# Kernel optimization log

Measured on AMD Instinct MI355X. Metric: run time of the kernel, lower is better.

Reference implementation:

```python
import jax, jax.numpy as jnp
import numpy as np

N = 100000
E = 1_600_000
IN_CH = 64
HID = 32       # per-head hidden dim
HEADS = 4
OUT_CH = 6
NEG_SLOPE = 0.2


def _glorot(key, shape):
    fan_in, fan_out = shape[0], shape[-1]
    lim = jnp.sqrt(6.0 / (fan_in + fan_out))
    return jax.random.uniform(key, shape, jnp.float32, -lim, lim)


def setup_inputs() -> dict:
    key = jax.random.key(0)
    ks = jax.random.split(key, 20)
    x = jax.random.normal(ks[0], (N, IN_CH), jnp.float32)
    edge_index = jax.random.randint(ks[1], (2, E), 0, N, jnp.int64)
    batch = jnp.zeros((N,), jnp.int64)
    inp = {"x": x, "edge_index": edge_index, "batch": batch}
    inp["W0"] = _glorot(ks[2], (IN_CH, HEADS * HID))
    inp["as0"] = _glorot(ks[3], (HEADS, HID))
    inp["ad0"] = _glorot(ks[4], (HEADS, HID))
    inp["b0"] = jnp.zeros((HEADS * HID,), jnp.float32)
    inp["W1"] = _glorot(ks[5], (HEADS * HID, HEADS * HID))
    inp["as1"] = _glorot(ks[6], (HEADS, HID))
    inp["ad1"] = _glorot(ks[7], (HEADS, HID))
    inp["b1"] = jnp.zeros((HEADS * HID,), jnp.float32)
    inp["W2"] = _glorot(ks[8], (HEADS * HID, HEADS * HID))
    inp["as2"] = _glorot(ks[9], (HEADS, HID))
    inp["ad2"] = _glorot(ks[10], (HEADS, HID))
    inp["b2"] = jnp.zeros((HEADS * HID,), jnp.float32)
    # final layer: 128 -> 6, 1 head, no concat (mean)
    inp["W3"] = _glorot(ks[11], (HEADS * HID, OUT_CH))
    inp["as3"] = _glorot(ks[12], (1, OUT_CH))
    inp["ad3"] = _glorot(ks[13], (1, OUT_CH))
    inp["b3"] = jnp.zeros((OUT_CH,), jnp.float32)
    return inp


def gat_conv(x, src, dst, W, a_src, a_dst, b, heads, concat):
    """PyG GATConv: linear -> per-edge attention -> segment softmax over dst -> scatter-add."""
    n = x.shape[0]
    h = (x @ W).reshape(n, heads, -1)                       # [N,H,D]
    al_s = jnp.sum(h * a_src, axis=-1)                      # [N,H]
    al_d = jnp.sum(h * a_dst, axis=-1)                      # [N,H]
    e = jax.nn.leaky_relu(al_s[src] + al_d[dst], NEG_SLOPE)  # [E,H]
    m = jax.ops.segment_max(e, dst, num_segments=n)         # segment softmax (stable)
    ex = jnp.exp(e - m[dst])
    s = jax.ops.segment_sum(ex, dst, num_segments=n)
    alpha = ex / (s[dst] + 1e-16)                           # [E,H]
    out = jax.ops.segment_sum(alpha[:, :, None] * h[src], dst, num_segments=n)  # [N,H,D]
    out = out.reshape(n, -1) if concat else out.mean(axis=1)
    return out + b


def reference(x, edge_index, batch, W0, as0, ad0, b0, W1, as1, ad1, b1,
              W2, as2, ad2, b2, W3, as3, ad3, b3):
    n = x.shape[0]
    # PyG GATConv adds self-loops by default; edge set is static (no pooling), add once.
    ar = jnp.arange(n, dtype=edge_index.dtype)
    ei = jnp.concatenate([edge_index, jnp.stack([ar, ar])], axis=1)
    src, dst = ei[0], ei[1]
    x = jax.nn.elu(gat_conv(x, src, dst, W0, as0, ad0, b0, HEADS, True))
    x = jax.nn.elu(gat_conv(x, src, dst, W1, as1, ad1, b1, HEADS, True))
    x = jax.nn.elu(gat_conv(x, src, dst, W2, as2, ad2, b2, HEADS, True))
    x = gat_conv(x, src, dst, W3, as3, ad3, b3, 1, False)   # final layer: no activation
    return x
```

## Files before the change

kernel.cpp:

```cpp
#include <hip/hip_runtime.h>
#include <hip/hip_bf16.h>
#include <hip/hip_fp16.h>

#define IN_CH 64
#define HID 32
#define HEADS 4
#define OUT_CH 6
#define NEG_SLOPE 0.2f


#define PBLK 256
#define CAP 6144

__global__ __launch_bounds__(256) void part_count(const int* __restrict__ ei, int E, int EN,
                                                  int NB, int epb, int* __restrict__ counts) {
    __shared__ int cnt[512];
    int b = blockIdx.x, t = threadIdx.x;
    for (int i = t; i < NB; i += 256) cnt[i] = 0;
    __syncthreads();
    int e0 = b * epb;
    int e1 = min(e0 + epb, EN);
    for (int e = e0 + t; e < e1; e += 256) {
        int d = (e < E) ? ei[E + e] : (e - E);
        atomicAdd(&cnt[d >> 8], 1);
    }
    __syncthreads();
    for (int i = t; i < NB; i += 256) counts[(size_t)i * PBLK + b] = cnt[i];
}

__global__ __launch_bounds__(256) void bucket_tot(const int* __restrict__ counts,
                                                  int* __restrict__ btot) {
    __shared__ int red[256];
    int k = blockIdx.x, t = threadIdx.x;
    red[t] = counts[(size_t)k * PBLK + t];
    __syncthreads();
    for (int off = 128; off; off >>= 1) {
        if (t < off) red[t] += red[t + off];
        __syncthreads();
    }
    if (t == 0) btot[k] = red[0];
}

__global__ __launch_bounds__(256) void bucket_scan(const int* __restrict__ btot, int NB, int EN,
                                                   int* __restrict__ bstart) {
    __shared__ int tmp[256];
    int t = threadIdx.x;
    int chunk = (NB + 255) >> 8;
    int s0 = t * chunk, s1 = min(s0 + chunk, NB);
    int sum = 0;
    for (int i = s0; i < s1; ++i) sum += btot[i];
    tmp[t] = sum;
    __syncthreads();
    for (int off = 1; off < 256; off <<= 1) {
        int v = (t >= off) ? tmp[t - off] : 0;
        __syncthreads();
        tmp[t] += v;
        __syncthreads();
    }
    int run = (t == 0) ? 0 : tmp[t - 1];
    for (int i = s0; i < s1; ++i) {
        int c = btot[i];
        bstart[i] = run;
        run += c;
    }
    if (t == 255) bstart[NB] = EN;
}

__global__ __launch_bounds__(256) void bucket_base(int* __restrict__ counts,
                                                   const int* __restrict__ bstart) {
    __shared__ int sc[256];
    int k = blockIdx.x, t = threadIdx.x;
    int v = counts[(size_t)k * PBLK + t];
    sc[t] = v;
    __syncthreads();
    for (int off = 1; off < 256; off <<= 1) {
        int u = (t >= off) ? sc[t - off] : 0;
        __syncthreads();
        sc[t] += u;
        __syncthreads();
    }
    counts[(size_t)k * PBLK + t] = bstart[k] + sc[t] - v;
}

__global__ __launch_bounds__(256) void part_scatter(const int* __restrict__ ei, int E, int EN,
                                                    int NB, int epb,
                                                    const int* __restrict__ base,
                                                    int2* __restrict__ ebuf) {
    __shared__ int cur[512];
    int b = blockIdx.x, t = threadIdx.x;
    for (int i = t; i < NB; i += 256) cur[i] = base[(size_t)i * PBLK + b];
    __syncthreads();
    int e0 = b * epb;
    int e1 = min(e0 + epb, EN);
    for (int e = e0 + t; e < e1; e += 256) {
        int s, d;
        if (e < E) { s = ei[e]; d = ei[E + e]; }
        else       { s = e - E; d = s; }
        int slot = atomicAdd(&cur[d >> 8], 1);
        ebuf[slot] = make_int2(s, d & 255);
    }
}

__global__ __launch_bounds__(256) void bucket_csr(const int2* __restrict__ ebuf,
                                                  const int* __restrict__ bstart,
                                                  int NB, int N, int EN,
                                                  int* __restrict__ row_start,
                                                  int* __restrict__ csr_src) {
    __shared__ int cnt[256];
    __shared__ int sc[256];
    __shared__ int stage[CAP];
    int k = blockIdx.x, t = threadIdx.x;
    int s0 = bstart[k], s1 = bstart[k + 1];
    int len = s1 - s0;
    cnt[t] = 0;
    __syncthreads();
    for (int i = t; i < len; i += 256) atomicAdd(&cnt[ebuf[s0 + i].y], 1);
    __syncthreads();
    int v = cnt[t];
    sc[t] = v;
    __syncthreads();
    for (int off = 1; off < 256; off <<= 1) {
        int u = (t >= off) ? sc[t - off] : 0;
        __syncthreads();
        sc[t] += u;
        __syncthreads();
    }
    int excl = sc[t] - v;
    int g = (k << 8) + t;
    if (g < N) row_start[g] = s0 + excl;
    if (k == NB - 1 && t == 0) row_start[N] = EN;
    bool fits = (len <= CAP);
    cnt[t] = fits ? excl : s0 + excl;
    __syncthreads();
    if (fits) {
        for (int i = t; i < len; i += 256) {
            int2 e = ebuf[s0 + i];
            int slot = atomicAdd(&cnt[e.y], 1);
            stage[slot] = e.x;
        }
        __syncthreads();
        for (int i = t; i < len; i += 256) csr_src[s0 + i] = stage[i];
    } else {
        for (int i = t; i < len; i += 256) {
            int2 e = ebuf[s0 + i];
            int slot = atomicAdd(&cnt[e.y], 1);
            csr_src[slot] = e.x;
        }
    }
}


#define BM 32
#define BKK 32

__global__ __launch_bounds__(256) void gemm128_kernel(const float* __restrict__ A,
                                                      const float* __restrict__ W,
                                                      const float* __restrict__ avs,
                                                      const float* __restrict__ avd,
                                                      __half* __restrict__ C,
                                                      float* __restrict__ als,
                                                      float* __restrict__ ald,
                                                      int N, int K) {
    __shared__ float xs[BM][BKK + 1];
    __shared__ float ws[BKK][128];
    __shared__ float red_s[BM][9];
    __shared__ float red_d[BM][9];
    int tid = threadIdx.x;
    int r  = tid & 31;
    int cg = tid >> 5;
    int row0 = blockIdx.x * BM;

    float acc[16];
#pragma unroll
    for (int j = 0; j < 16; ++j) acc[j] = 0.f;

    for (int kk = 0; kk < K; kk += BKK) {
        {
            int lr = tid >> 3, lc = (tid & 7) * 4;
            int gr = row0 + lr;
            float4 v = make_float4(0.f, 0.f, 0.f, 0.f);
            if (gr < N) v = *reinterpret_cast<const float4*>(A + (size_t)gr * K + kk + lc);
            xs[lr][lc + 0] = v.x; xs[lr][lc + 1] = v.y;
            xs[lr][lc + 2] = v.z; xs[lr][lc + 3] = v.w;
        }
        {
            int wr = tid >> 3, wc = (tid & 7) * 16;
            const float4* src = reinterpret_cast<const float4*>(W + (size_t)(kk + wr) * 128 + wc);
            float4* dst = reinterpret_cast<float4*>(&ws[wr][wc]);
#pragma unroll
            for (int i = 0; i < 4; ++i) dst[i] = src[i];
        }
        __syncthreads();
#pragma unroll 8
        for (int k = 0; k < BKK; ++k) {
            float xv = xs[r][k];
            const float4* wrow = reinterpret_cast<const float4*>(&ws[k][cg * 16]);
#pragma unroll
            for (int q = 0; q < 4; ++q) {
                float4 wv = wrow[q];
                acc[q * 4 + 0] += xv * wv.x;
                acc[q * 4 + 1] += xv * wv.y;
                acc[q * 4 + 2] += xv * wv.z;
                acc[q * 4 + 3] += xv * wv.w;
            }
        }
        __syncthreads();
    }
    int gr = row0 + r;
    if (gr < N) {
        __half2* outp = reinterpret_cast<__half2*>(C + (size_t)gr * 128 + cg * 16);
#pragma unroll
        for (int q = 0; q < 8; ++q)
            outp[q] = __float22half2_rn(make_float2(acc[q * 2], acc[q * 2 + 1]));
    }
    {
        float ps = 0.f, pd = 0.f;
#pragma unroll
        for (int q = 0; q < 16; ++q) {
            float a = acc[q];
            ps += a * avs[cg * 16 + q];
            pd += a * avd[cg * 16 + q];
        }
        red_s[r][cg] = ps;
        red_d[r][cg] = pd;
        __syncthreads();
        if (gr < N) {
            if (cg < 4) {
                als[(size_t)gr * 4 + cg] = red_s[r][2 * cg] + red_s[r][2 * cg + 1];
            } else {
                int hd = cg - 4;
                ald[(size_t)gr * 4 + hd] = red_d[r][2 * hd] + red_d[r][2 * hd + 1];
            }
        }
    }
}


__device__ __forceinline__ float lrelu(float x) { return x > 0.f ? x : NEG_SLOPE * x; }

__global__ __launch_bounds__(256) void agg_kernel(const __half* __restrict__ h,
                                                  const float* __restrict__ als4,
                                                  const float* __restrict__ ald4,
                                                  const int* __restrict__ row_start,
                                                  const int* __restrict__ csr_src,
                                                  const float* __restrict__ bias,
                                                  float* __restrict__ xout,
                                                  int N, int applyElu) {
    int v = (int)((blockIdx.x * blockDim.x + threadIdx.x) >> 6);
    int lane = threadIdx.x & 63;
    if (v >= N) return;
    int base = row_start[v], end = row_start[v + 1];

    int half_ = lane >> 5;
    int dim4 = (lane & 31) * 4;
    int hd2  = (lane & 31) >> 3;

    float aldh = ald4[(size_t)v * 4 + hd2];
    float alsh = als4[(size_t)v * 4 + hd2];
    float em = lrelu(alsh + aldh);
    const __half* hdim = h + dim4;
    const float* alsb = als4 + hd2;

    float4 acc  = make_float4(0.f, 0.f, 0.f, 0.f);
    float4 acc2 = make_float4(0.f, 0.f, 0.f, 0.f);
    float ssum = 0.f, ssum2 = 0.f;

    int j = base + half_;
    for (; j + 6 < end; j += 8) {
        int s0 = csr_src[j + 0];
        int s1 = csr_src[j + 2];
        int s2 = csr_src[j + 4];
        int s3 = csr_src[j + 6];
        float a0 = alsb[(size_t)s0 * 4];
        float a1 = alsb[(size_t)s1 * 4];
        float a2 = alsb[(size_t)s2 * 4];
        float a3 = alsb[(size_t)s3 * 4];
        uint2 r0 = *reinterpret_cast<const uint2*>(hdim + (size_t)s0 * 128);
        uint2 r1 = *reinterpret_cast<const uint2*>(hdim + (size_t)s1 * 128);
        uint2 r2 = *reinterpret_cast<const uint2*>(hdim + (size_t)s2 * 128);
        uint2 r3 = *reinterpret_cast<const uint2*>(hdim + (size_t)s3 * 128);
        float e0 = __expf(lrelu(a0 + aldh) - em);
        float e1 = __expf(lrelu(a1 + aldh) - em);
        float e2 = __expf(lrelu(a2 + aldh) - em);
        float e3 = __expf(lrelu(a3 + aldh) - em);
        ssum  += e0 + e2;
        ssum2 += e1 + e3;
        float2 f0a = __half22float2(*reinterpret_cast<__half2*>(&r0.x));
        float2 f0b = __half22float2(*reinterpret_cast<__half2*>(&r0.y));
        float2 f1a = __half22float2(*reinterpret_cast<__half2*>(&r1.x));
        float2 f1b = __half22float2(*reinterpret_cast<__half2*>(&r1.y));
        float2 f2a = __half22float2(*reinterpret_cast<__half2*>(&r2.x));
        float2 f2b = __half22float2(*reinterpret_cast<__half2*>(&r2.y));
        float2 f3a = __half22float2(*reinterpret_cast<__half2*>(&r3.x));
        float2 f3b = __half22float2(*reinterpret_cast<__half2*>(&r3.y));
        acc.x  += e0 * f0a.x; acc.y  += e0 * f0a.y; acc.z  += e0 * f0b.x; acc.w  += e0 * f0b.y;
        acc2.x += e1 * f1a.x; acc2.y += e1 * f1a.y; acc2.z += e1 * f1b.x; acc2.w += e1 * f1b.y;
        acc.x  += e2 * f2a.x; acc.y  += e2 * f2a.y; acc.z  += e2 * f2b.x; acc.w  += e2 * f2b.y;
        acc2.x += e3 * f3a.x; acc2.y += e3 * f3a.y; acc2.z += e3 * f3b.x; acc2.w += e3 * f3b.y;
    }
    for (; j < end; j += 2) {
        int s0 = csr_src[j];
        float a0 = alsb[(size_t)s0 * 4];
        uint2 r0 = *reinterpret_cast<const uint2*>(hdim + (size_t)s0 * 128);
        float e0 = __expf(lrelu(a0 + aldh) - em);
        ssum += e0;
        float2 f0a = __half22float2(*reinterpret_cast<__half2*>(&r0.x));
        float2 f0b = __half22float2(*reinterpret_cast<__half2*>(&r0.y));
        acc.x += e0 * f0a.x; acc.y += e0 * f0a.y; acc.z += e0 * f0b.x; acc.w += e0 * f0b.y;
    }
    acc.x += acc2.x; acc.y += acc2.y; acc.z += acc2.z; acc.w += acc2.w;
    ssum += ssum2;
    acc.x += __shfl_xor(acc.x, 32);
    acc.y += __shfl_xor(acc.y, 32);
    acc.z += __shfl_xor(acc.z, 32);
    acc.w += __shfl_xor(acc.w, 32);
    ssum  += __shfl_xor(ssum, 32);

    if (lane < 32) {
        float inv = 1.0f / (ssum + 1e-16f);
        float4 bv = *reinterpret_cast<const float4*>(bias + dim4);
        float4 o;
        o.x = acc.x * inv + bv.x;
        o.y = acc.y * inv + bv.y;
        o.z = acc.z * inv + bv.z;
        o.w = acc.w * inv + bv.w;
        if (applyElu) {
            o.x = o.x > 0.f ? o.x : expm1f(o.x);
            o.y = o.y > 0.f ? o.y : expm1f(o.y);
            o.z = o.z > 0.f ? o.z : expm1f(o.z);
            o.w = o.w > 0.f ? o.w : expm1f(o.w);
        }
        *reinterpret_cast<float4*>(xout + (size_t)v * 128 + dim4) = o;
    }
}


__global__ void gemm3_kernel(const float* __restrict__ x, const float* __restrict__ W,
                             const float* __restrict__ as3, const float* __restrict__ ad3,
                             float* __restrict__ h3, float* __restrict__ als3,
                             float* __restrict__ ald3, int N) {
    int n = blockIdx.x * blockDim.x + threadIdx.x;
    if (n >= N) return;
    float acc[6] = {0.f, 0.f, 0.f, 0.f, 0.f, 0.f};
    const float4* xp = reinterpret_cast<const float4*>(x + (size_t)n * 128);
#pragma unroll 4
    for (int k4 = 0; k4 < 32; ++k4) {
        float4 xv = xp[k4];
        const float* w0 = W + (size_t)(k4 * 4) * 6;
#pragma unroll
        for (int j = 0; j < 6; ++j)
            acc[j] += xv.x * w0[j] + xv.y * w0[6 + j] + xv.z * w0[12 + j] + xv.w * w0[18 + j];
    }
    float s = 0.f, d = 0.f;
#pragma unroll
    for (int j = 0; j < 6; ++j) {
        s += acc[j] * as3[j];
        d += acc[j] * ad3[j];
        h3[(size_t)n * 6 + j] = acc[j];
    }
    als3[n] = s;
    ald3[n] = d;
}

__global__ void agg3_kernel(const float* __restrict__ h3, const float* __restrict__ als3,
                            const float* __restrict__ ald3, const int* __restrict__ row_start,
                            const int* __restrict__ csr_src, const float* __restrict__ b3,
                            float* __restrict__ out, int N) {
    int v = blockIdx.x * blockDim.x + threadIdx.x;
    if (v >= N) return;
    int base = row_start[v], end = row_start[v + 1];
    float aldv = ald3[v];
    float em = lrelu(als3[v] + aldv);
    float ssum = 0.f;
    float acc[6] = {0.f, 0.f, 0.f, 0.f, 0.f, 0.f};
    float acc2[6] = {0.f, 0.f, 0.f, 0.f, 0.f, 0.f};
    int j = base;
    for (; j + 1 < end; j += 2) {
        int sa = csr_src[j], sb = csr_src[j + 1];
        float ea = __expf(lrelu(als3[sa] + aldv) - em);
        float eb = __expf(lrelu(als3[sb] + aldv) - em);
        ssum += ea + eb;
        const float* ha = h3 + (size_t)sa * 6;
        const float* hb = h3 + (size_t)sb * 6;
#pragma unroll
        for (int q = 0; q < 6; ++q) acc[q] += ea * ha[q];
#pragma unroll
        for (int q = 0; q < 6; ++q) acc2[q] += eb * hb[q];
    }
    if (j < end) {
        int sa = csr_src[j];
        float ea = __expf(lrelu(als3[sa] + aldv) - em);
        ssum += ea;
        const float* ha = h3 + (size_t)sa * 6;
#pragma unroll
        for (int q = 0; q < 6; ++q) acc[q] += ea * ha[q];
    }
    float inv = 1.f / (ssum + 1e-16f);
#pragma unroll
    for (int q = 0; q < 6; ++q) out[(size_t)v * 6 + q] = (acc[q] + acc2[q]) * inv + b3[q];
}


extern "C" void kernel_launch(void* const* d_in, const int* in_sizes, int n_in,
                              void* d_out, int out_size, void* d_ws, size_t ws_size,
                              hipStream_t stream) {
    const float* x    = (const float*)d_in[0];
    const int*   ei   = (const int*)d_in[1];
    const float* W0   = (const float*)d_in[3];
    const float* as0  = (const float*)d_in[4];
    const float* ad0  = (const float*)d_in[5];
    const float* b0   = (const float*)d_in[6];
    const float* W1   = (const float*)d_in[7];
    const float* as1  = (const float*)d_in[8];
    const float* ad1  = (const float*)d_in[9];
    const float* b1   = (const float*)d_in[10];
    const float* W2   = (const float*)d_in[11];
    const float* as2  = (const float*)d_in[12];
    const float* ad2  = (const float*)d_in[13];
    const float* b2   = (const float*)d_in[14];
    const float* W3   = (const float*)d_in[15];
    const float* as3  = (const float*)d_in[16];
    const float* ad3  = (const float*)d_in[17];
    const float* b3   = (const float*)d_in[18];
    float* out = (float*)d_out;

    int N = in_sizes[0] / IN_CH;
    int E = in_sizes[1] / 2;
    int EN = E + N;
    int NB = (N + 255) >> 8;
    int epb = (EN + PBLK - 1) / PBLK;

    char* p = (char*)d_ws;
    auto alloc = [&](size_t bytes) {
        char* q = p;
        p += (bytes + 255) & ~(size_t)255;
        return q;
    };
    __half* hbuf = (__half*)alloc((size_t)N * 128 * 2);
    float* xA   = (float*)alloc((size_t)N * 128 * 4);
    float* xB   = (float*)alloc((size_t)N * 128 * 4);
    float* als  = (float*)alloc((size_t)N * 4 * 4);
    float* ald  = (float*)alloc((size_t)N * 4 * 4);
    float* h3   = (float*)alloc((size_t)N * 6 * 4);
    float* als3 = (float*)alloc((size_t)N * 4);
    float* ald3 = (float*)alloc((size_t)N * 4);
    int* row_start = (int*)alloc((size_t)(N + 1) * 4);
    int* csr_src   = (int*)alloc((size_t)EN * 4);
    int2* ebuf     = (int2*)alloc((size_t)EN * 8);
    int* counts    = (int*)alloc((size_t)NB * PBLK * 4);
    int* btot      = (int*)alloc((size_t)NB * 4);
    int* bstart    = (int*)alloc((size_t)(NB + 1) * 4);
    (void)ws_size; (void)n_in; (void)out_size;

    part_count<<<PBLK, 256, 0, stream>>>(ei, E, EN, NB, epb, counts);
    bucket_tot<<<NB, 256, 0, stream>>>(counts, btot);
    bucket_scan<<<1, 256, 0, stream>>>(btot, NB, EN, bstart);
    bucket_base<<<NB, 256, 0, stream>>>(counts, bstart);
    part_scatter<<<PBLK, 256, 0, stream>>>(ei, E, EN, NB, epb, counts, ebuf);
    bucket_csr<<<NB, 256, 0, stream>>>(ebuf, bstart, NB, N, EN, row_start, csr_src);

    int gemm_grid = (N + BM - 1) / BM;
    int agg_grid  = (N + 3) / 4;
    int n_grid    = (N + 255) / 256;

    gemm128_kernel<<<gemm_grid, 256, 0, stream>>>(x, W0, as0, ad0, hbuf, als, ald, N, 64);
    agg_kernel<<<agg_grid, 256, 0, stream>>>(hbuf, als, ald, row_start, csr_src, b0, xA, N, 1);

    gemm128_kernel<<<gemm_grid, 256, 0, stream>>>(xA, W1, as1, ad1, hbuf, als, ald, N, 128);
    agg_kernel<<<agg_grid, 256, 0, stream>>>(hbuf, als, ald, row_start, csr_src, b1, xB, N, 1);

    gemm128_kernel<<<gemm_grid, 256, 0, stream>>>(xB, W2, as2, ad2, hbuf, als, ald, N, 128);
    agg_kernel<<<agg_grid, 256, 0, stream>>>(hbuf, als, ald, row_start, csr_src, b2, xA, N, 1);

    gemm3_kernel<<<n_grid, 256, 0, stream>>>(xA, W3, as3, ad3, h3, als3, ald3, N);
    agg3_kernel<<<n_grid, 256, 0, stream>>>(h3, als3, ald3, row_start, csr_src, b3, out, N);
}
```

Measured before the change: 521.5 us.

## Use 8x4 register tiles and transposed A tile in 128-wide GEMM

Reworks the node-feature GEMM so each thread computes an 8-row by 4-column register tile over a 64-row block, with the A tile stored transposed in shared memory for vectorised float4 reads. The attention-logit reductions now use warp shuffles instead of a shared-memory reduction and an extra barrier. The aim is more FMAs per shared-memory load and a lower LDS-to-compute ratio. The trade-off is higher register pressure and fewer blocks, since the block now covers 64 rows.

New measurement: 458.2 us. 1.14x faster.

```diff
diff --git a/kernel.cpp b/kernel.cpp
--- a/kernel.cpp
+++ b/kernel.cpp
@@ -150,8 +150,9 @@
 }
 
 
-#define BM 32
-#define BKK 32
+#define GBM 64
+#define GBK 32
+#define XST 68
 
 __global__ __launch_bounds__(256) void gemm128_kernel(const float* __restrict__ A,
                                                       const float* __restrict__ W,
@@ -161,75 +162,91 @@
                                                       float* __restrict__ als,
                                                       float* __restrict__ ald,
                                                       int N, int K) {
-    __shared__ float xs[BM][BKK + 1];
-    __shared__ float ws[BKK][128];
-    __shared__ float red_s[BM][9];
-    __shared__ float red_d[BM][9];
+    __shared__ float xsT[GBK][XST];
+    __shared__ float ws[GBK][128];
     int tid = threadIdx.x;
-    int r  = tid & 31;
-    int cg = tid >> 5;
-    int row0 = blockIdx.x * BM;
-
-    float acc[16];
-#pragma unroll
-    for (int j = 0; j < 16; ++j) acc[j] = 0.f;
-
-    for (int kk = 0; kk < K; kk += BKK) {
+    int rt = tid >> 5;
+    int ct = tid & 31;
+    int row0 = blockIdx.x * GBM;
+
+    float acc[8][4];
+#pragma unroll
+    for (int i = 0; i < 8; ++i)
+#pragma unroll
+        for (int j = 0; j < 4; ++j) acc[i][j] = 0.f;
+
+    int arow = tid & 63;
+    int acg  = (tid >> 6) * 8;
+    int garow = row0 + arow;
+
+    for (int kk = 0; kk < K; kk += GBK) {
         {
-            int lr = tid >> 3, lc = (tid & 7) * 4;
-            int gr = row0 + lr;
-            float4 v = make_float4(0.f, 0.f, 0.f, 0.f);
-            if (gr < N) v = *reinterpret_cast<const float4*>(A + (size_t)gr * K + kk + lc);
-            xs[lr][lc + 0] = v.x; xs[lr][lc + 1] = v.y;
-            xs[lr][lc + 2] = v.z; xs[lr][lc + 3] = v.w;
+            float4 a0 = make_float4(0.f, 0.f, 0.f, 0.f);
+            float4 a1 = make_float4(0.f, 0.f, 0.f, 0.f);
+            if (garow < N) {
+                const float4* ap = reinterpret_cast<const float4*>(A + (size_t)garow * K + kk + acg);
+                a0 = ap[0]; a1 = ap[1];
+            }
+            xsT[acg + 0][arow] = a0.x; xsT[acg + 1][arow] = a0.y;
+            xsT[acg + 2][arow] = a0.z; xsT[acg + 3][arow] = a0.w;
+            xsT[acg + 4][arow] = a1.x; xsT[acg + 5][arow] = a1.y;
+            xsT[acg + 6][arow] = a1.z; xsT[acg + 7][arow] = a1.w;
         }
         {
-            int wr = tid >> 3, wc = (tid & 7) * 16;
-            const float4* src = reinterpret_cast<const float4*>(W + (size_t)(kk + wr) * 128 + wc);
-            float4* dst = reinterpret_cast<float4*>(&ws[wr][wc]);
-#pragma unroll
-            for (int i = 0; i < 4; ++i) dst[i] = src[i];
-        }
-        __syncthreads();
-#pragma unroll 8
-        for (int k = 0; k < BKK; ++k) {
-            float xv = xs[r][k];
-            const float4* wrow = reinterpret_cast<const float4*>(&ws[k][cg * 16]);
-#pragma unroll
-            for (int q = 0; q < 4; ++q) {
-                float4 wv = wrow[q];
-                acc[q * 4 + 0] += xv * wv.x;
-                acc[q * 4 + 1] += xv * wv.y;
-                acc[q * 4 + 2] += xv * wv.z;
-                acc[q * 4 + 3] += xv * wv.w;
+            float4* wflat = reinterpret_cast<float4*>(&ws[0][0]);
+            const float4* wsrc = reinterpret_cast<const float4*>(W + (size_t)kk * 128);
+#pragma unroll
+            for (int c = 0; c < 4; ++c) {
+                int p = tid + 256 * c;
+                wflat[p] = wsrc[p];
             }
         }
         __syncthreads();
-    }
-    int gr = row0 + r;
-    if (gr < N) {
-        __half2* outp = reinterpret_cast<__half2*>(C + (size_t)gr * 128 + cg * 16);
-#pragma unroll
-        for (int q = 0; q < 8; ++q)
-            outp[q] = __float22half2_rn(make_float2(acc[q * 2], acc[q * 2 + 1]));
-    }
-    {
-        float ps = 0.f, pd = 0.f;
-#pragma unroll
-        for (int q = 0; q < 16; ++q) {
-            float a = acc[q];
-            ps += a * avs[cg * 16 + q];
-            pd += a * avd[cg * 16 + q];
-        }
-        red_s[r][cg] = ps;
-        red_d[r][cg] = pd;
-        __syncthreads();
+#pragma unroll 4
+        for (int k = 0; k < GBK; ++k) {
+            float4 av0 = *reinterpret_cast<const float4*>(&xsT[k][rt * 8]);
+            float4 av1 = *reinterpret_cast<const float4*>(&xsT[k][rt * 8 + 4]);
+            float4 wv  = *reinterpret_cast<const float4*>(&ws[k][ct * 4]);
+            acc[0][0] += av0.x * wv.x; acc[0][1] += av0.x * wv.y; acc[0][2] += av0.x * wv.z; acc[0][3] += av0.x * wv.w;
+            acc[1][0] += av0.y * wv.x; acc[1][1] += av0.y * wv.y; acc[1][2] += av0.y * wv.z; acc[1][3] += av0.y * wv.w;
+            acc[2][0] += av0.z * wv.x; acc[2][1] += av0.z * wv.y; acc[2][2] += av0.z * wv.z; acc[2][3] += av0.z * wv.w;
+            acc[3][0] += av0.w * wv.x; acc[3][1] += av0.w * wv.y; acc[3][2] += av0.w * wv.z; acc[3][3] += av0.w * wv.w;
+            acc[4][0] += av1.x * wv.x; acc[4][1] += av1.x * wv.y; acc[4][2] += av1.x * wv.z; acc[4][3] += av1.x * wv.w;
+            acc[5][0] += av1.y * wv.x; acc[5][1] += av1.y * wv.y; acc[5][2] += av1.y * wv.z; acc[5][3] += av1.y * wv.w;
+            acc[6][0] += av1.z * wv.x; acc[6][1] += av1.z * wv.y; acc[6][2] += av1.z * wv.z; acc[6][3] += av1.z * wv.w;
+            acc[7][0] += av1.w * wv.x; acc[7][1] += av1.w * wv.y; acc[7][2] += av1.w * wv.z; acc[7][3] += av1.w * wv.w;
+        }
+        __syncthreads();
+    }
+
+#pragma unroll
+    for (int i = 0; i < 8; ++i) {
+        int gr = row0 + rt * 8 + i;
         if (gr < N) {
-            if (cg < 4) {
-                als[(size_t)gr * 4 + cg] = red_s[r][2 * cg] + red_s[r][2 * cg + 1];
-            } else {
-                int hd = cg - 4;
-                ald[(size_t)gr * 4 + hd] = red_d[r][2 * hd] + red_d[r][2 * hd + 1];
+            __half2* outp = reinterpret_cast<__half2*>(C + (size_t)gr * 128 + ct * 4);
+            outp[0] = __float22half2_rn(make_float2(acc[i][0], acc[i][1]));
+            outp[1] = __float22half2_rn(make_float2(acc[i][2], acc[i][3]));
+        }
+    }
+    float avs_c[4], avd_c[4];
+#pragma unroll
+    for (int j = 0; j < 4; ++j) {
+        avs_c[j] = avs[ct * 4 + j];
+        avd_c[j] = avd[ct * 4 + j];
+    }
+#pragma unroll
+    for (int i = 0; i < 8; ++i) {
+        float ps = acc[i][0] * avs_c[0] + acc[i][1] * avs_c[1] + acc[i][2] * avs_c[2] + acc[i][3] * avs_c[3];
+        float pd = acc[i][0] * avd_c[0] + acc[i][1] * avd_c[1] + acc[i][2] * avd_c[2] + acc[i][3] * avd_c[3];
+        ps += __shfl_xor(ps, 1); pd += __shfl_xor(pd, 1);
+        ps += __shfl_xor(ps, 2); pd += __shfl_xor(pd, 2);
+        ps += __shfl_xor(ps, 4); pd += __shfl_xor(pd, 4);
+        if ((ct & 7) == 0) {
+            int gr = row0 + rt * 8 + i;
+            int hd = ct >> 3;
+            if (gr < N) {
+                als[(size_t)gr * 4 + hd] = ps;
+                ald[(size_t)gr * 4 + hd] = pd;
             }
         }
     }
@@ -459,7 +476,7 @@
     part_scatter<<<PBLK, 256, 0, stream>>>(ei, E, EN, NB, epb, counts, ebuf);
     bucket_csr<<<NB, 256, 0, stream>>>(ebuf, bstart, NB, N, EN, row_start, csr_src);
 
-    int gemm_grid = (N + BM - 1) / BM;
+    int gemm_grid = (N + GBM - 1) / GBM;
     int agg_grid  = (N + 3) / 4;
     int n_grid    = (N + 255) / 256;
 
```

## Use fp16 MFMA for node-feature GEMMs and store activations in half precision

Applied to the files above, without the earlier changes.

Replaces the fp32 scalar-FMA GEMM with a 16x16x32 fp16 MFMA kernel. Each wave loads its A-fragments straight from global memory and reads weights that a small kernel has pre-transposed and converted to fp16. Aggregation outputs and the layer-0 input are now stored in fp16, which halves activation traffic for the GEMMs and for gemm3. The attention logit dot products are reduced with wave shuffles. This costs extra precision loss, a few small conversion kernels, and uncoalesced scalar fp16 stores of C.

After: 445.8 us. -14.5%, faster.

```diff
diff --git a/kernel.cpp b/kernel.cpp
--- a/kernel.cpp
+++ b/kernel.cpp
@@ -7,6 +7,9 @@
 #define HEADS 4
 #define OUT_CH 6
 #define NEG_SLOPE 0.2f
+
+typedef __attribute__((ext_vector_type(8))) _Float16 half8;
+typedef __attribute__((ext_vector_type(4))) float f32x4;
 
 
 #define PBLK 256
@@ -150,86 +153,122 @@
 }
 
 
-#define BM 32
-#define BKK 32
-
-__global__ __launch_bounds__(256) void gemm128_kernel(const float* __restrict__ A,
-                                                      const float* __restrict__ W,
-                                                      const float* __restrict__ avs,
-                                                      const float* __restrict__ avd,
-                                                      __half* __restrict__ C,
-                                                      float* __restrict__ als,
-                                                      float* __restrict__ ald,
-                                                      int N, int K) {
-    __shared__ float xs[BM][BKK + 1];
-    __shared__ float ws[BKK][128];
-    __shared__ float red_s[BM][9];
-    __shared__ float red_d[BM][9];
+__global__ void xconv_kernel(const float* __restrict__ x, __half* __restrict__ xh, int total4) {
+    int t = blockIdx.x * blockDim.x + threadIdx.x;
+    if (t >= total4) return;
+    float4 v = *reinterpret_cast<const float4*>(x + (size_t)t * 4);
+    __half2* op = reinterpret_cast<__half2*>(xh + (size_t)t * 4);
+    op[0] = __float22half2_rn(make_float2(v.x, v.y));
+    op[1] = __float22half2_rn(make_float2(v.z, v.w));
+}
+
+__global__ void wtrans_kernel(const float* __restrict__ W, __half* __restrict__ WT,
+                              int K, int kshift) {
+    int o = blockIdx.x * blockDim.x + threadIdx.x;
+    if (o >= (K << 7)) return;
+    int c = o >> kshift;
+    int k = o & (K - 1);
+    WT[o] = __float2half(W[(size_t)k * 128 + c]);
+}
+
+
+__global__ __launch_bounds__(256) void gemm_mfma(const __half* __restrict__ A,
+                                                 const __half* __restrict__ WT,
+                                                 const float* __restrict__ avs,
+                                                 const float* __restrict__ avd,
+                                                 __half* __restrict__ C,
+                                                 float* __restrict__ als,
+                                                 float* __restrict__ ald,
+                                                 int N, int K) {
     int tid = threadIdx.x;
-    int r  = tid & 31;
-    int cg = tid >> 5;
-    int row0 = blockIdx.x * BM;
-
-    float acc[16];
-#pragma unroll
-    for (int j = 0; j < 16; ++j) acc[j] = 0.f;
-
-    for (int kk = 0; kk < K; kk += BKK) {
-        {
-            int lr = tid >> 3, lc = (tid & 7) * 4;
-            int gr = row0 + lr;
-            float4 v = make_float4(0.f, 0.f, 0.f, 0.f);
-            if (gr < N) v = *reinterpret_cast<const float4*>(A + (size_t)gr * K + kk + lc);
-            xs[lr][lc + 0] = v.x; xs[lr][lc + 1] = v.y;
-            xs[lr][lc + 2] = v.z; xs[lr][lc + 3] = v.w;
-        }
-        {
-            int wr = tid >> 3, wc = (tid & 7) * 16;
-            const float4* src = reinterpret_cast<const float4*>(W + (size_t)(kk + wr) * 128 + wc);
-            float4* dst = reinterpret_cast<float4*>(&ws[wr][wc]);
-#pragma unroll
-            for (int i = 0; i < 4; ++i) dst[i] = src[i];
-        }
-        __syncthreads();
-#pragma unroll 8
-        for (int k = 0; k < BKK; ++k) {
-            float xv = xs[r][k];
-            const float4* wrow = reinterpret_cast<const float4*>(&ws[k][cg * 16]);
-#pragma unroll
-            for (int q = 0; q < 4; ++q) {
-                float4 wv = wrow[q];
-                acc[q * 4 + 0] += xv * wv.x;
-                acc[q * 4 + 1] += xv * wv.y;
-                acc[q * 4 + 2] += xv * wv.z;
-                acc[q * 4 + 3] += xv * wv.w;
+    int wv = tid >> 6, lane = tid & 63;
+    int row0 = blockIdx.x * 64 + wv * 16;
+    int lrow = lane & 15;
+    int lk = (lane >> 4) * 8;
+    int garow = row0 + lrow;
+
+    half8 afrag[4];
+#pragma unroll
+    for (int ks = 0; ks < 4; ++ks) {
+        half8 z = {(_Float16)0, (_Float16)0, (_Float16)0, (_Float16)0,
+                   (_Float16)0, (_Float16)0, (_Float16)0, (_Float16)0};
+        afrag[ks] = z;
+    }
+    if (garow < N) {
+        const __half* ap = A + (size_t)garow * K + lk;
+        if (K == 128) {
+#pragma unroll
+            for (int ks = 0; ks < 4; ++ks)
+                afrag[ks] = *reinterpret_cast<const half8*>(ap + ks * 32);
+        } else {
+#pragma unroll
+            for (int ks = 0; ks < 2; ++ks)
+                afrag[ks] = *reinterpret_cast<const half8*>(ap + ks * 32);
+        }
+    }
+
+    f32x4 acc[8];
+#pragma unroll
+    for (int t = 0; t < 8; ++t) acc[t] = (f32x4){0.f, 0.f, 0.f, 0.f};
+
+#pragma unroll
+    for (int t = 0; t < 8; ++t) {
+        const __half* wb = WT + (size_t)(t * 16 + lrow) * K + lk;
+        if (K == 128) {
+#pragma unroll
+            for (int ks = 0; ks < 4; ++ks) {
+                half8 bfrag = *reinterpret_cast<const half8*>(wb + ks * 32);
+                acc[t] = __builtin_amdgcn_mfma_f32_16x16x32_f16(afrag[ks], bfrag, acc[t], 0, 0, 0);
             }
-        }
-        __syncthreads();
-    }
-    int gr = row0 + r;
-    if (gr < N) {
-        __half2* outp = reinterpret_cast<__half2*>(C + (size_t)gr * 128 + cg * 16);
-#pragma unroll
-        for (int q = 0; q < 8; ++q)
-            outp[q] = __float22half2_rn(make_float2(acc[q * 2], acc[q * 2 + 1]));
-    }
-    {
-        float ps = 0.f, pd = 0.f;
-#pragma unroll
-        for (int q = 0; q < 16; ++q) {
-            float a = acc[q];
-            ps += a * avs[cg * 16 + q];
-            pd += a * avd[cg * 16 + q];
-        }
-        red_s[r][cg] = ps;
-        red_d[r][cg] = pd;
-        __syncthreads();
-        if (gr < N) {
-            if (cg < 4) {
-                als[(size_t)gr * 4 + cg] = red_s[r][2 * cg] + red_s[r][2 * cg + 1];
-            } else {
-                int hd = cg - 4;
-                ald[(size_t)gr * 4 + hd] = red_d[r][2 * hd] + red_d[r][2 * hd + 1];
+        } else {
+#pragma unroll
+            for (int ks = 0; ks < 2; ++ks) {
+                half8 bfrag = *reinterpret_cast<const half8*>(wb + ks * 32);
+                acc[t] = __builtin_amdgcn_mfma_f32_16x16x32_f16(afrag[ks], bfrag, acc[t], 0, 0, 0);
+            }
+        }
+    }
+
+    int rbase = (lane >> 4) * 4;
+#pragma unroll
+    for (int t = 0; t < 8; ++t) {
+#pragma unroll
+        for (int j = 0; j < 4; ++j) {
+            int gr = row0 + rbase + j;
+            if (gr < N) C[(size_t)gr * 128 + t * 16 + lrow] = __float2half(acc[t][j]);
+        }
+    }
+    float ps[4][4], pd[4][4];
+#pragma unroll
+    for (int h = 0; h < 4; ++h)
+#pragma unroll
+        for (int j = 0; j < 4; ++j) { ps[h][j] = 0.f; pd[h][j] = 0.f; }
+#pragma unroll
+    for (int t = 0; t < 8; ++t) {
+        int ht = t >> 1;
+        float as_c = avs[t * 16 + lrow];
+        float ad_c = avd[t * 16 + lrow];
+#pragma unroll
+        for (int j = 0; j < 4; ++j) {
+            ps[ht][j] += acc[t][j] * as_c;
+            pd[ht][j] += acc[t][j] * ad_c;
+        }
+    }
+#pragma unroll
+    for (int h = 0; h < 4; ++h) {
+#pragma unroll
+        for (int j = 0; j < 4; ++j) {
+            float s = ps[h][j], d = pd[h][j];
+            s += __shfl_xor(s, 1); d += __shfl_xor(d, 1);
+            s += __shfl_xor(s, 2); d += __shfl_xor(d, 2);
+            s += __shfl_xor(s, 4); d += __shfl_xor(d, 4);
+            s += __shfl_xor(s, 8); d += __shfl_xor(d, 8);
+            if (lrow == 0) {
+                int gr = row0 + rbase + j;
+                if (gr < N) {
+                    als[(size_t)gr * 4 + h] = s;
+                    ald[(size_t)gr * 4 + h] = d;
+                }
             }
         }
     }
@@ -244,7 +283,7 @@
                                                   const int* __restrict__ row_start,
                                                   const int* __restrict__ csr_src,
                                                   const float* __restrict__ bias,
-                                                  float* __restrict__ xout,
+                                                  __half* __restrict__ xout,
                                                   int N, int applyElu) {
     int v = (int)((blockIdx.x * blockDim.x + threadIdx.x) >> 6);
     int lane = threadIdx.x & 63;
@@ -330,33 +369,42 @@
             o.z = o.z > 0.f ? o.z : expm1f(o.z);
             o.w = o.w > 0.f ? o.w : expm1f(o.w);
         }
-        *reinterpret_cast<float4*>(xout + (size_t)v * 128 + dim4) = o;
-    }
-}
-
-
-__global__ void gemm3_kernel(const float* __restrict__ x, const float* __restrict__ W,
+        __half2* op = reinterpret_cast<__half2*>(xout + (size_t)v * 128 + dim4);
+        op[0] = __float22half2_rn(make_float2(o.x, o.y));
+        op[1] = __float22half2_rn(make_float2(o.z, o.w));
+    }
+}
+
+
+__global__ void gemm3_kernel(const __half* __restrict__ x, const float* __restrict__ W,
                              const float* __restrict__ as3, const float* __restrict__ ad3,
                              float* __restrict__ h3, float* __restrict__ als3,
                              float* __restrict__ ald3, int N) {
     int n = blockIdx.x * blockDim.x + threadIdx.x;
     if (n >= N) return;
     float acc[6] = {0.f, 0.f, 0.f, 0.f, 0.f, 0.f};
-    const float4* xp = reinterpret_cast<const float4*>(x + (size_t)n * 128);
-#pragma unroll 4
-    for (int k4 = 0; k4 < 32; ++k4) {
-        float4 xv = xp[k4];
-        const float* w0 = W + (size_t)(k4 * 4) * 6;
-#pragma unroll
-        for (int j = 0; j < 6; ++j)
-            acc[j] += xv.x * w0[j] + xv.y * w0[6 + j] + xv.z * w0[12 + j] + xv.w * w0[18 + j];
+    const __half* xp = x + (size_t)n * 128;
+#pragma unroll 2
+    for (int k8 = 0; k8 < 16; ++k8) {
+        uint4 rv = *reinterpret_cast<const uint4*>(xp + k8 * 8);
+        float2 fa = __half22float2(*reinterpret_cast<__half2*>(&rv.x));
+        float2 fb = __half22float2(*reinterpret_cast<__half2*>(&rv.y));
+        float2 fc = __half22float2(*reinterpret_cast<__half2*>(&rv.z));
+        float2 fd = __half22float2(*reinterpret_cast<__half2*>(&rv.w));
+        float xv[8] = {fa.x, fa.y, fb.x, fb.y, fc.x, fc.y, fd.x, fd.y};
+        const float* w0 = W + (size_t)(k8 * 8) * 6;
+#pragma unroll
+        for (int kk = 0; kk < 8; ++kk)
+#pragma unroll
+            for (int q = 0; q < 6; ++q)
+                acc[q] += xv[kk] * w0[kk * 6 + q];
     }
     float s = 0.f, d = 0.f;
 #pragma unroll
-    for (int j = 0; j < 6; ++j) {
-        s += acc[j] * as3[j];
-        d += acc[j] * ad3[j];
-        h3[(size_t)n * 6 + j] = acc[j];
+    for (int q = 0; q < 6; ++q) {
+        s += acc[q] * as3[q];
+        d += acc[q] * ad3[q];
+        h3[(size_t)n * 6 + q] = acc[q];
     }
     als3[n] = s;
     ald3[n] = d;
@@ -436,9 +484,13 @@
         p += (bytes + 255) & ~(size_t)255;
         return q;
     };
+    __half* xh   = (__half*)alloc((size_t)N * 64 * 2);
     __half* hbuf = (__half*)alloc((size_t)N * 128 * 2);
-    float* xA   = (float*)alloc((size_t)N * 128 * 4);
-    float* xB   = (float*)alloc((size_t)N * 128 * 4);
+    __half* xA   = (__half*)alloc((size_t)N * 128 * 2);
+    __half* xB   = (__half*)alloc((size_t)N * 128 * 2);
+    __half* WT0  = (__half*)alloc((size_t)128 * 64 * 2);
+    __half* WT1  = (__half*)alloc((size_t)128 * 128 * 2);
+    __half* WT2  = (__half*)alloc((size_t)128 * 128 * 2);
     float* als  = (float*)alloc((size_t)N * 4 * 4);
     float* ald  = (float*)alloc((size_t)N * 4 * 4);
     float* h3   = (float*)alloc((size_t)N * 6 * 4);
@@ -459,17 +511,22 @@
     part_scatter<<<PBLK, 256, 0, stream>>>(ei, E, EN, NB, epb, counts, ebuf);
     bucket_csr<<<NB, 256, 0, stream>>>(ebuf, bstart, NB, N, EN, row_start, csr_src);
 
-    int gemm_grid = (N + BM - 1) / BM;
+    xconv_kernel<<<(N * 16 + 255) / 256, 256, 0, stream>>>(x, xh, N * 16);
+    wtrans_kernel<<<(128 * 64 + 255) / 256, 256, 0, stream>>>(W0, WT0, 64, 6);
+    wtrans_kernel<<<(128 * 128 + 255) / 256, 256, 0, stream>>>(W1, WT1, 128, 7);
+    wtrans_kernel<<<(128 * 128 + 255) / 256, 256, 0, stream>>>(W2, WT2, 128, 7);
+
+    int gemm_grid = (N + 63) / 64;
     int agg_grid  = (N + 3) / 4;
     int n_grid    = (N + 255) / 256;
 
-    gemm128_kernel<<<gemm_grid, 256, 0, stream>>>(x, W0, as0, ad0, hbuf, als, ald, N, 64);
+    gemm_mfma<<<gemm_grid, 256, 0, stream>>>(xh, WT0, as0, ad0, hbuf, als, ald, N, 64);
     agg_kernel<<<agg_grid, 256, 0, stream>>>(hbuf, als, ald, row_start, csr_src, b0, xA, N, 1);
 
-    gemm128_kernel<<<gemm_grid, 256, 0, stream>>>(xA, W1, as1, ad1, hbuf, als, ald, N, 128);
+    gemm_mfma<<<gemm_grid, 256, 0, stream>>>(xA, WT1, as1, ad1, hbuf, als, ald, N, 128);
     agg_kernel<<<agg_grid, 256, 0, stream>>>(hbuf, als, ald, row_start, csr_src, b1, xB, N, 1);
 
-    gemm128_kernel<<<gemm_grid, 256, 0, stream>>>(xB, W2, as2, ad2, hbuf, als, ald, N, 128);
+    gemm_mfma<<<gemm_grid, 256, 0, stream>>>(xB, WT2, as2, ad2, hbuf, als, ald, N, 128);
     agg_kernel<<<agg_grid, 256, 0, stream>>>(hbuf, als, ald, row_start, csr_src, b2, xA, N, 1);
 
     gemm3_kernel<<<n_grid, 256, 0, stream>>>(xA, W3, as3, ad3, h3, als3, ald3, N);
```
